# Optimization experiments

Measured on AMD Instinct MI355X. Metric: run time of the kernel, lower is better.

The kernel has to match this reference:

```python
import jax, jax.numpy as jnp
import numpy as np

D = 1024   # dim == seq_len L (forced by final proj on [L, L])
N = 16     # SSM state size
K = 3      # conv kernel size, padding=1 -> same length


def setup_inputs() -> dict:
    key = jax.random.key(0)
    ks = jax.random.split(key, 8)
    s = lambda k, shape, sc: (jax.random.normal(k, shape, jnp.float32) * sc)
    return {
        "x": s(ks[0], (2, D, D), 1.0),
        "W_proj": s(ks[1], (D, D), D ** -0.5),
        "b_proj": jnp.zeros((D,), jnp.float32),
        "conv_w": s(ks[2], (D, D, K), (D * K) ** -0.5),  # [out_ch, in_ch, K]
        "conv_b": jnp.zeros((D,), jnp.float32),
        "A_log": jnp.log(jnp.tile(jnp.arange(1, N + 1, dtype=jnp.float32)[None, :], (D, 1))),  # [D, N]
        "W_delta": s(ks[3], (D, D), D ** -0.5),
        "W_B": s(ks[4], (D, N), D ** -0.5),
        "W_C": s(ks[5], (D, N), D ** -0.5),
    }


def _ssm(x, A_log, W_delta, W_B, W_C):
    # Mamba S6 diagonal selective scan. x: [L, D]
    delta = jax.nn.softplus(x @ W_delta)            # [L, D]
    B = x @ W_B                                      # [L, N]
    C = x @ W_C                                      # [L, N]
    A = -jnp.exp(A_log)                              # [D, N]
    Abar = jnp.exp(delta[:, :, None] * A[None])      # [L, D, N]
    Bx = (delta * x)[:, :, None] * B[:, None, :]     # [L, D, N]

    def combine(e1, e2):
        a1, b1 = e1
        a2, b2 = e2
        return a1 * a2, a2 * b1 + b2

    _, h = jax.lax.associative_scan(combine, (Abar, Bx), axis=0)  # h: [L, D, N]
    return jnp.einsum('ldn,ln->ld', h, C)            # [L, D]


def reference(x, W_proj, b_proj, conv_w, conv_b, A_log, W_delta, W_B, W_C):
    p = x @ W_proj.T + b_proj                        # shared proj; [2, L, D]
    xm, xg = p[0], p[1]                              # mirrors `x, x_ = self.proj(x)` unpacking batch==2
    xg = jax.nn.silu(xg)                             # [L, D]
    # Conv1d treats xm as (channels=L, length=D), padding=1 -> same length
    xc = jax.lax.conv_general_dilated(
        xm[None], conv_w, window_strides=(1,), padding=[(1, 1)],
        dimension_numbers=('NCW', 'OIW', 'NCW'))[0] + conv_b[:, None]  # [L, D]
    xc = jax.nn.silu(xc)
    y = _ssm(xc, A_log, W_delta, W_B, W_C)           # [L, D]
    y = y @ xg.T                                     # [L, L]  (x @ x_.transpose(-1,-2))
    return y @ W_proj.T + b_proj                     # final shared proj; [L, L]
```

## Files before the change

### kernel.cpp

```cpp
#include <hip/hip_runtime.h>
#include <math.h>


#define LL 1024
#define DD 1024
#define NS 16
#define CCH 16
#define CLEN 64

typedef short     bf16x8_t __attribute__((ext_vector_type(8)));
typedef float     f32x4_t  __attribute__((ext_vector_type(4)));
typedef unsigned short u16x4_t __attribute__((ext_vector_type(4)));
typedef unsigned short u16x8_t __attribute__((ext_vector_type(8)));

__device__ __forceinline__ float silu_f(float x) { return x / (1.f + expf(-x)); }
__device__ __forceinline__ float softplus_f(float x) {
  return fmaxf(x, 0.f) + log1pf(expf(-fabsf(x)));
}
__device__ __forceinline__ unsigned short f2bf(float f) {
  unsigned int u = __float_as_uint(f);
  u += 0x7fffu + ((u >> 16) & 1u);
  return (unsigned short)(u >> 16);
}

template<int N> __device__ __forceinline__ void s_wait_vmcnt() {
  asm volatile("s_waitcnt vmcnt(%0)" :: "n"(N) : "memory");
}
__device__ __forceinline__ void raw_barrier() {
  asm volatile("s_barrier" ::: "memory");
}

__global__ __launch_bounds__(256) void castk(const float* __restrict__ in,
                                             unsigned short* __restrict__ out, int n) {
  int i = (blockIdx.x * 256 + threadIdx.x) * 4;
  if (i >= n) return;
  float4 v = *(const float4*)(in + i);
  u16x4_t o; o[0] = f2bf(v.x); o[1] = f2bf(v.y); o[2] = f2bf(v.z); o[3] = f2bf(v.w);
  *(u16x4_t*)(out + i) = o;
}

__global__ __launch_bounds__(256) void tcastk(const float* __restrict__ W,
                                              unsigned short* __restrict__ out) {
  __shared__ float T[64][65];
  const int t = threadIdx.x;
  const int r = t >> 2, cq = (t & 3) << 4;
  const int d0 = blockIdx.x * 64, k0 = blockIdx.y * 64;
  #pragma unroll
  for (int c = 0; c < 16; c += 4) {
    float4 v = *(const float4*)&W[(size_t)(k0 + r) * DD + d0 + cq + c];
    T[r][cq + c + 0] = v.x; T[r][cq + c + 1] = v.y;
    T[r][cq + c + 2] = v.z; T[r][cq + c + 3] = v.w;
  }
  __syncthreads();
  u16x8_t o0, o1;
  #pragma unroll
  for (int j = 0; j < 8; ++j) o0[j] = f2bf(T[cq + j][r]);
  #pragma unroll
  for (int j = 0; j < 8; ++j) o1[j] = f2bf(T[cq + 8 + j][r]);
  *(u16x8_t*)&out[(size_t)(d0 + r) * DD + k0 + cq] = o0;
  *(u16x8_t*)&out[(size_t)(d0 + r) * DD + k0 + cq + 8] = o1;
}

__global__ __launch_bounds__(256) void bct_cast(const float* __restrict__ WB,
                                                const float* __restrict__ WC,
                                                unsigned short* __restrict__ wcomb) {
  const int b = blockIdx.x;
  const int k = threadIdx.x * 4;
  u16x4_t o;
  if (b < 32) {
    const float* W = (b < 16) ? WB : WC;
    const int n = b & 15;
    #pragma unroll
    for (int j = 0; j < 4; ++j) o[j] = f2bf(W[(size_t)(k + j) * NS + n]);
  } else {
    o[0] = o[1] = o[2] = o[3] = 0;
  }
  *(u16x4_t*)&wcomb[(size_t)(1024 + b) * DD + k] = o;
}

__global__ __launch_bounds__(256) void transpose_f32(const float* __restrict__ in,
                                                     float* __restrict__ out) {
  __shared__ float T[64][65];
  const int t = threadIdx.x;
  const int r = t >> 4;
  const int cq = (t & 15) << 2;
  const int r0 = blockIdx.y * 64, c0 = blockIdx.x * 64;
  #pragma unroll
  for (int rr = 0; rr < 64; rr += 16) {
    float4 v = *(const float4*)&in[(size_t)(r0 + r + rr) * DD + c0 + cq];
    T[r + rr][cq + 0] = v.x; T[r + rr][cq + 1] = v.y;
    T[r + rr][cq + 2] = v.z; T[r + rr][cq + 3] = v.w;
  }
  __syncthreads();
  #pragma unroll
  for (int rr = 0; rr < 64; rr += 16) {
    float4 o;
    o.x = T[cq + 0][r + rr]; o.y = T[cq + 1][r + rr];
    o.z = T[cq + 2][r + rr]; o.w = T[cq + 3][r + rr];
    *(float4*)&out[(size_t)(c0 + r + rr) * LL + r0 + cq] = o;
  }
}

__global__ __launch_bounds__(256) void build_xsht(const unsigned short* __restrict__ xm,
                                                  unsigned short* __restrict__ out) {
  __shared__ unsigned short Xs[64][66];
  const int t = threadIdx.x;
  const int w0 = blockIdx.x * 64, i0 = blockIdx.y * 64;
  {
    const int r = t >> 2, cq = (t & 3) << 4;
    #pragma unroll
    for (int c = 0; c < 16; c += 4) {
      u16x4_t v = *(const u16x4_t*)&xm[(size_t)(i0 + r) * DD + w0 + cq + c];
      Xs[r][1 + cq + c + 0] = v[0]; Xs[r][1 + cq + c + 1] = v[1];
      Xs[r][1 + cq + c + 2] = v[2]; Xs[r][1 + cq + c + 3] = v[3];
    }
  }
  if (t < 64)                 Xs[t][0]       = (w0 > 0)        ? xm[(size_t)(i0 + t) * DD + w0 - 1]  : (unsigned short)0;
  else if (t < 128) { int r = t - 64; Xs[r][65] = (w0 + 64 < DD) ? xm[(size_t)(i0 + r) * DD + w0 + 64] : (unsigned short)0; }
  __syncthreads();
  const int wr = t >> 2, q = t & 3;
  unsigned short vals[48];
  #pragma unroll
  for (int ii = 0; ii < 16; ++ii)
    #pragma unroll
    for (int k = 0; k < 3; ++k)
      vals[ii * 3 + k] = Xs[q * 16 + ii][wr + k];
  #pragma unroll
  for (int s = 0; s < 6; ++s) {
    u16x8_t o;
    #pragma unroll
    for (int j = 0; j < 8; ++j) o[j] = vals[s * 8 + j];
    *(u16x8_t*)&out[(size_t)(w0 + wr) * 3072 + (size_t)i0 * 3 + q * 48 + s * 8] = o;
  }
}

template<int TM, int NC, int ACT, bool BROW, bool O32, bool O16>
__global__ __launch_bounds__(256) void gemm_bf16(
    const unsigned short* __restrict__ A, const unsigned short* __restrict__ B,
    const float* __restrict__ bias, float* __restrict__ C32,
    unsigned short* __restrict__ C16, int M, int N, int K)
{
  constexpr int MI   = TM / 32;
  constexpr int NI   = NC / 32;
  constexpr int ROWS = TM + NC;
  constexpr int GI   = ROWS * 8 / 256;
  __shared__ unsigned short s[3][ROWS * 64];
  const int tid  = threadIdx.x;
  const int lane = tid & 63;
  const int wv   = tid >> 6;
  const int wm   = wv >> 1, wn = wv & 1;
  const int m0 = blockIdx.y * TM, n0 = blockIdx.x * NC;
  const int wbase = tid & 192;

  f32x4_t acc[MI][NI];
  #pragma unroll
  for (int i = 0; i < MI; ++i)
    #pragma unroll
    for (int j = 0; j < NI; ++j)
      acc[i][j] = (f32x4_t)(0.f);

  auto stage = [&](int buf, int k0) {
    #pragma unroll
    for (int it = 0; it < GI; ++it) {
      const int c   = (it << 8) + tid;
      const int r   = c >> 3;
      const int kcg = (c & 7) ^ (r & 7);
      const unsigned short* src = (r < TM)
          ? (A + (size_t)(m0 + r) * K + k0 + kcg * 8)
          : (B + (size_t)(n0 + r - TM) * K + k0 + kcg * 8);
      __builtin_amdgcn_global_load_lds(
          (const __attribute__((address_space(1))) void*)src,
          (__attribute__((address_space(3))) void*)(&s[buf][0] + (size_t)((it << 8) + wbase) * 8),
          16, 0, 0);
    }
  };

  const int NT = K >> 6;
  stage(0, 0);
  stage(1, 64);
  s_wait_vmcnt<GI>();
  raw_barrier();

  for (int t = 0; t < NT; ++t) {
    if (t + 2 < NT) stage((t + 2) % 3, (t + 2) << 6);

    const unsigned short* sb = &s[t % 3][0];
    const int rl = lane & 15, kq = lane >> 4;
    bf16x8_t af[MI][2], bfr[NI][2];
    #pragma unroll
    for (int mi = 0; mi < MI; ++mi) {
      const int row = wm * (TM / 2) + mi * 16 + rl;
      #pragma unroll
      for (int ks = 0; ks < 2; ++ks) {
        const int ch = row * 8 + ((ks * 4 + kq) ^ (row & 7));
        af[mi][ks] = *(const bf16x8_t*)(sb + (size_t)ch * 8);
      }
    }
    #pragma unroll
    for (int ni = 0; ni < NI; ++ni) {
      const int row = TM + wn * (NC / 2) + ni * 16 + rl;
      #pragma unroll
      for (int ks = 0; ks < 2; ++ks) {
        const int ch = row * 8 + ((ks * 4 + kq) ^ (row & 7));
        bfr[ni][ks] = *(const bf16x8_t*)(sb + (size_t)ch * 8);
      }
    }
    #pragma unroll
    for (int mi = 0; mi < MI; ++mi)
      #pragma unroll
      for (int ni = 0; ni < NI; ++ni)
        #pragma unroll
        for (int ks = 0; ks < 2; ++ks)
          acc[mi][ni] = __builtin_amdgcn_mfma_f32_16x16x32_bf16(
              af[mi][ks], bfr[ni][ks], acc[mi][ni], 0, 0, 0);

    if (t + 1 < NT) {
      if (t + 2 < NT) s_wait_vmcnt<GI>();
      else            s_wait_vmcnt<0>();
      raw_barrier();
    }
  }

  const int rl = lane & 15, rg = lane >> 4;
  #pragma unroll
  for (int mi = 0; mi < MI; ++mi) {
    #pragma unroll
    for (int ni = 0; ni < NI; ++ni) {
      const int col = n0 + wn * (NC / 2) + ni * 16 + rl;
      #pragma unroll
      for (int j = 0; j < 4; ++j) {
        const int row = m0 + wm * (TM / 2) + mi * 16 + rg * 4 + j;
        float v = acc[mi][ni][j];
        if (bias) v += BROW ? bias[row] : bias[col];
        if (ACT == 1) v = silu_f(v);
        else if (ACT == 2) v = softplus_f(v);
        else if (ACT == 3) { if (row >= 1024) v = silu_f(v); }
        else if (ACT == 4) { if (row < 1024)  v = softplus_f(v); }
        if (O32) C32[(size_t)row * N + col] = v;
        if (O16) C16[(size_t)row * N + col] = f2bf(v);
      }
    }
  }
}

__global__ __launch_bounds__(256) void scan_p1(
    const float* __restrict__ deltaT, const float* __restrict__ xcT,
    const float* __restrict__ BT, const float* __restrict__ A_log,
    float* __restrict__ P, float* __restrict__ H)
{
  const int tid = threadIdx.x;
  const int n = tid & 15, dl = tid >> 4;
  const int d = blockIdx.y * 16 + dl;
  const int c = blockIdx.x;
  const int l0 = c * CLEN;
  const float Av = -expf(A_log[d * NS + n]);
  float h = 0.f, p = 1.f;
  for (int j = 0; j < CLEN; j += 4) {
    const float4 dv = *(const float4*)&deltaT[(size_t)d * LL + l0 + j];
    const float4 xv = *(const float4*)&xcT[(size_t)d * LL + l0 + j];
    const float4 bv = *(const float4*)&BT[(size_t)n * LL + l0 + j];
    const float dvu[4] = {dv.x, dv.y, dv.z, dv.w};
    const float xvu[4] = {xv.x, xv.y, xv.z, xv.w};
    const float bvu[4] = {bv.x, bv.y, bv.z, bv.w};
    #pragma unroll
    for (int u = 0; u < 4; ++u) {
      const float ab = expf(dvu[u] * Av);
      h = fmaf(ab, h, dvu[u] * xvu[u] * bvu[u]);
      p *= ab;
    }
  }
  const int idx = d * NS + n;
  P[(size_t)c * (DD * NS) + idx] = p;
  H[(size_t)c * (DD * NS) + idx] = h;
}

__global__ __launch_bounds__(256) void scan_p2(const float* __restrict__ P,
                                               const float* __restrict__ H,
                                               float* __restrict__ Hin) {
  const int idx = blockIdx.x * 256 + threadIdx.x;
  float hin = 0.f;
  Hin[idx] = 0.f;
  #pragma unroll
  for (int c = 1; c < CCH; ++c) {
    hin = fmaf(P[(size_t)(c - 1) * (DD * NS) + idx], hin,
               H[(size_t)(c - 1) * (DD * NS) + idx]);
    Hin[(size_t)c * (DD * NS) + idx] = hin;
  }
}

__global__ __launch_bounds__(256) void scan_p3(
    const float* __restrict__ deltaT, const float* __restrict__ xcT,
    const float* __restrict__ BT, const float* __restrict__ CT,
    const float* __restrict__ Hin, const float* __restrict__ A_log,
    unsigned short* __restrict__ y16)
{
  const int tid = threadIdx.x;
  const int n = tid & 15, dl = tid >> 4;
  const int d = blockIdx.y * 16 + dl;
  const int c = blockIdx.x;
  const int l0 = c * CLEN;
  const float Av = -expf(A_log[d * NS + n]);
  float h = Hin[(size_t)c * (DD * NS) + d * NS + n];
  for (int j = 0; j < CLEN; j += 4) {
    const float4 dv = *(const float4*)&deltaT[(size_t)d * LL + l0 + j];
    const float4 xv = *(const float4*)&xcT[(size_t)d * LL + l0 + j];
    const float4 bv = *(const float4*)&BT[(size_t)n * LL + l0 + j];
    const float4 cv = *(const float4*)&CT[(size_t)n * LL + l0 + j];
    const float dvu[4] = {dv.x, dv.y, dv.z, dv.w};
    const float xvu[4] = {xv.x, xv.y, xv.z, xv.w};
    const float bvu[4] = {bv.x, bv.y, bv.z, bv.w};
    const float cvu[4] = {cv.x, cv.y, cv.z, cv.w};
    #pragma unroll
    for (int u = 0; u < 4; ++u) {
      const int l = l0 + j + u;
      const float ab = expf(dvu[u] * Av);
      h = fmaf(ab, h, dvu[u] * xvu[u] * bvu[u]);
      float contrib = h * cvu[u];
      contrib += __shfl_xor(contrib, 1);
      contrib += __shfl_xor(contrib, 2);
      contrib += __shfl_xor(contrib, 4);
      contrib += __shfl_xor(contrib, 8);
      if (n == 0) y16[(size_t)l * DD + d] = f2bf(contrib);
    }
  }
}

extern "C" void kernel_launch(void* const* d_in, const int* in_sizes, int n_in,
                              void* d_out, int out_size, void* d_ws, size_t ws_size,
                              hipStream_t stream) {
  const float* x       = (const float*)d_in[0];
  const float* W_proj  = (const float*)d_in[1];
  const float* b_proj  = (const float*)d_in[2];
  const float* conv_w  = (const float*)d_in[3];
  const float* conv_b  = (const float*)d_in[4];
  const float* A_log   = (const float*)d_in[5];
  const float* W_delta = (const float*)d_in[6];
  const float* W_B     = (const float*)d_in[7];
  const float* W_C     = (const float*)d_in[8];
  float* out = (float*)d_out;

  char* w = (char*)d_ws;
  const size_t MB = 1024 * 1024;
  unsigned short* x16     = (unsigned short*)(w + 0);
  unsigned short* wp16    = (unsigned short*)(w + 4 * MB);
  unsigned short* cw16    = (unsigned short*)(w + 6 * MB);
  unsigned short* wcomb16 = (unsigned short*)(w + 12 * MB);
  unsigned short* pbuf    = (unsigned short*)(w + 15 * MB);
  unsigned short* xm16    = pbuf;
  unsigned short* xg16    = pbuf + 1024 * 1024;
  unsigned short* xsht    = (unsigned short*)(w + 19 * MB);
  unsigned short* xc16    = (unsigned short*)(w + 25 * MB);
  float*          xc32    = (float*)(w + 27 * MB);
  float*          xcT32   = (float*)(w + 31 * MB);
  float*          dcomb32 = (float*)(w + 35 * MB);
  float*          deltaT32= dcomb32;
  float*          BT32    = dcomb32 + (size_t)1024 * 1024;
  float*          CT32    = dcomb32 + (size_t)1040 * 1024;
  unsigned short* y16     = (unsigned short*)(w + 40 * MB);
  float*          Pc      = (float*)(w + 42 * MB);
  float*          Hc      = (float*)(w + 43 * MB);
  float*          HinC    = (float*)(w + 44 * MB);
  unsigned short* out116  = (unsigned short*)(w + 45 * MB);
  (void)ws_size;

  const dim3 blk(256);

  castk<<<dim3(2048), blk, 0, stream>>>(x, x16, 2 * 1024 * 1024);
  castk<<<dim3(1024), blk, 0, stream>>>(W_proj, wp16, 1024 * 1024);
  castk<<<dim3(3072), blk, 0, stream>>>(conv_w, cw16, 3 * 1024 * 1024);
  tcastk<<<dim3(16, 16), blk, 0, stream>>>(W_delta, wcomb16);
  bct_cast<<<dim3(64), blk, 0, stream>>>(W_B, W_C, wcomb16);

  gemm_bf16<64, 64, 3, false, false, true><<<dim3(16, 32), blk, 0, stream>>>(
      x16, wp16, b_proj, nullptr, pbuf, 2048, 1024, 1024);
  build_xsht<<<dim3(16, 16), blk, 0, stream>>>(xm16, xsht);
  gemm_bf16<64, 64, 1, true, true, true><<<dim3(16, 16), blk, 0, stream>>>(
      cw16, xsht, conv_b, xc32, xc16, 1024, 1024, 3072);
  gemm_bf16<64, 64, 4, false, true, false><<<dim3(16, 17), blk, 0, stream>>>(
      wcomb16, xc16, nullptr, dcomb32, nullptr, 1088, 1024, 1024);
  transpose_f32<<<dim3(16, 16), blk, 0, stream>>>(xc32, xcT32);
  scan_p1<<<dim3(CCH, DD / 16), blk, 0, stream>>>(deltaT32, xcT32, BT32, A_log, Pc, Hc);
  scan_p2<<<dim3(64), blk, 0, stream>>>(Pc, Hc, HinC);
  scan_p3<<<dim3(CCH, DD / 16), blk, 0, stream>>>(deltaT32, xcT32, BT32, CT32, HinC, A_log, y16);
  gemm_bf16<64, 64, 0, false, false, true><<<dim3(16, 16), blk, 0, stream>>>(
      y16, xg16, nullptr, nullptr, out116, 1024, 1024, 1024);
  gemm_bf16<64, 64, 0, false, true, false><<<dim3(16, 16), blk, 0, stream>>>(
      out116, wp16, b_proj, out, nullptr, 1024, 1024, 1024);
}
```

Measured before the change: 204.6 us.

## Replace 64x64 GEMMs with 128x128 split-K GEMMs plus fused reduction epilogues

```diff
diff --git a/kernel.cpp b/kernel.cpp
--- a/kernel.cpp
+++ b/kernel.cpp
@@ -78,29 +78,6 @@
   *(u16x4_t*)&wcomb[(size_t)(1024 + b) * DD + k] = o;
 }
 
-__global__ __launch_bounds__(256) void transpose_f32(const float* __restrict__ in,
-                                                     float* __restrict__ out) {
-  __shared__ float T[64][65];
-  const int t = threadIdx.x;
-  const int r = t >> 4;
-  const int cq = (t & 15) << 2;
-  const int r0 = blockIdx.y * 64, c0 = blockIdx.x * 64;
-  #pragma unroll
-  for (int rr = 0; rr < 64; rr += 16) {
-    float4 v = *(const float4*)&in[(size_t)(r0 + r + rr) * DD + c0 + cq];
-    T[r + rr][cq + 0] = v.x; T[r + rr][cq + 1] = v.y;
-    T[r + rr][cq + 2] = v.z; T[r + rr][cq + 3] = v.w;
-  }
-  __syncthreads();
-  #pragma unroll
-  for (int rr = 0; rr < 64; rr += 16) {
-    float4 o;
-    o.x = T[cq + 0][r + rr]; o.y = T[cq + 1][r + rr];
-    o.z = T[cq + 2][r + rr]; o.w = T[cq + 3][r + rr];
-    *(float4*)&out[(size_t)(c0 + r + rr) * LL + r0 + cq] = o;
-  }
-}
-
 __global__ __launch_bounds__(256) void build_xsht(const unsigned short* __restrict__ xm,
                                                   unsigned short* __restrict__ out) {
   __shared__ unsigned short Xs[64][66];
@@ -134,40 +111,36 @@
   }
 }
 
-template<int TM, int NC, int ACT, bool BROW, bool O32, bool O16>
-__global__ __launch_bounds__(256) void gemm_bf16(
+__global__ __launch_bounds__(256) void gemm_sk(
     const unsigned short* __restrict__ A, const unsigned short* __restrict__ B,
-    const float* __restrict__ bias, float* __restrict__ C32,
-    unsigned short* __restrict__ C16, int M, int N, int K)
+    float* __restrict__ part, size_t sliceStride, int N, int K, int Ksl)
 {
-  constexpr int MI   = TM / 32;
-  constexpr int NI   = NC / 32;
-  constexpr int ROWS = TM + NC;
-  constexpr int GI   = ROWS * 8 / 256;
-  __shared__ unsigned short s[3][ROWS * 64];
+  constexpr int GI = 4;
+  __shared__ unsigned short s[3][256 * 32];
   const int tid  = threadIdx.x;
   const int lane = tid & 63;
   const int wv   = tid >> 6;
   const int wm   = wv >> 1, wn = wv & 1;
-  const int m0 = blockIdx.y * TM, n0 = blockIdx.x * NC;
+  const int m0 = blockIdx.y * 128, n0 = blockIdx.x * 128;
   const int wbase = tid & 192;
-
-  f32x4_t acc[MI][NI];
-  #pragma unroll
-  for (int i = 0; i < MI; ++i)
-    #pragma unroll
-    for (int j = 0; j < NI; ++j)
+  const int koff = blockIdx.z * Ksl;
+
+  f32x4_t acc[4][4];
+  #pragma unroll
+  for (int i = 0; i < 4; ++i)
+    #pragma unroll
+    for (int j = 0; j < 4; ++j)
       acc[i][j] = (f32x4_t)(0.f);
 
-  auto stage = [&](int buf, int k0) {
+  auto stage = [&](int buf, int kbase) {
     #pragma unroll
     for (int it = 0; it < GI; ++it) {
       const int c   = (it << 8) + tid;
-      const int r   = c >> 3;
-      const int kcg = (c & 7) ^ (r & 7);
-      const unsigned short* src = (r < TM)
-          ? (A + (size_t)(m0 + r) * K + k0 + kcg * 8)
-          : (B + (size_t)(n0 + r - TM) * K + k0 + kcg * 8);
+      const int r   = c >> 2;
+      const int kcg = (c & 3) ^ ((r >> 1) & 3);
+      const unsigned short* src = (r < 128)
+          ? (A + (size_t)(m0 + r) * K + kbase + kcg * 8)
+          : (B + (size_t)(n0 + r - 128) * K + kbase + kcg * 8);
       __builtin_amdgcn_global_load_lds(
           (const __attribute__((address_space(1))) void*)src,
           (__attribute__((address_space(3))) void*)(&s[buf][0] + (size_t)((it << 8) + wbase) * 8),
@@ -175,44 +148,35 @@
     }
   };
 
-  const int NT = K >> 6;
-  stage(0, 0);
-  stage(1, 64);
+  const int NT = Ksl >> 5;
+  stage(0, koff);
+  stage(1, koff + 32);
   s_wait_vmcnt<GI>();
   raw_barrier();
 
   for (int t = 0; t < NT; ++t) {
-    if (t + 2 < NT) stage((t + 2) % 3, (t + 2) << 6);
+    if (t + 2 < NT) stage((t + 2) % 3, koff + (t + 2) * 32);
 
     const unsigned short* sb = &s[t % 3][0];
     const int rl = lane & 15, kq = lane >> 4;
-    bf16x8_t af[MI][2], bfr[NI][2];
-    #pragma unroll
-    for (int mi = 0; mi < MI; ++mi) {
-      const int row = wm * (TM / 2) + mi * 16 + rl;
+    bf16x8_t af[4], bfr[4];
+    #pragma unroll
+    for (int mi = 0; mi < 4; ++mi) {
+      const int row = wm * 64 + mi * 16 + rl;
+      const int ch  = row * 4 + (kq ^ ((row >> 1) & 3));
+      af[mi] = *(const bf16x8_t*)(sb + (size_t)ch * 8);
+    }
+    #pragma unroll
+    for (int ni = 0; ni < 4; ++ni) {
+      const int row = 128 + wn * 64 + ni * 16 + rl;
+      const int ch  = row * 4 + (kq ^ ((row >> 1) & 3));
+      bfr[ni] = *(const bf16x8_t*)(sb + (size_t)ch * 8);
+    }
+    #pragma unroll
+    for (int mi = 0; mi < 4; ++mi)
       #pragma unroll
-      for (int ks = 0; ks < 2; ++ks) {
-        const int ch = row * 8 + ((ks * 4 + kq) ^ (row & 7));
-        af[mi][ks] = *(const bf16x8_t*)(sb + (size_t)ch * 8);
-      }
-    }
-    #pragma unroll
-    for (int ni = 0; ni < NI; ++ni) {
-      const int row = TM + wn * (NC / 2) + ni * 16 + rl;
-      #pragma unroll
-      for (int ks = 0; ks < 2; ++ks) {
-        const int ch = row * 8 + ((ks * 4 + kq) ^ (row & 7));
-        bfr[ni][ks] = *(const bf16x8_t*)(sb + (size_t)ch * 8);
-      }
-    }
-    #pragma unroll
-    for (int mi = 0; mi < MI; ++mi)
-      #pragma unroll
-      for (int ni = 0; ni < NI; ++ni)
-        #pragma unroll
-        for (int ks = 0; ks < 2; ++ks)
-          acc[mi][ni] = __builtin_amdgcn_mfma_f32_16x16x32_bf16(
-              af[mi][ks], bfr[ni][ks], acc[mi][ni], 0, 0, 0);
+      for (int ni = 0; ni < 4; ++ni)
+        acc[mi][ni] = __builtin_amdgcn_mfma_f32_16x16x32_bf16(af[mi], bfr[ni], acc[mi][ni], 0, 0, 0);
 
     if (t + 1 < NT) {
       if (t + 2 < NT) s_wait_vmcnt<GI>();
@@ -221,25 +185,88 @@
     }
   }
 
+  float* pz = part + (size_t)blockIdx.z * sliceStride;
   const int rl = lane & 15, rg = lane >> 4;
   #pragma unroll
-  for (int mi = 0; mi < MI; ++mi) {
-    #pragma unroll
-    for (int ni = 0; ni < NI; ++ni) {
-      const int col = n0 + wn * (NC / 2) + ni * 16 + rl;
+  for (int mi = 0; mi < 4; ++mi) {
+    #pragma unroll
+    for (int ni = 0; ni < 4; ++ni) {
+      const int col = n0 + wn * 64 + ni * 16 + rl;
       #pragma unroll
       for (int j = 0; j < 4; ++j) {
-        const int row = m0 + wm * (TM / 2) + mi * 16 + rg * 4 + j;
-        float v = acc[mi][ni][j];
-        if (bias) v += BROW ? bias[row] : bias[col];
-        if (ACT == 1) v = silu_f(v);
-        else if (ACT == 2) v = softplus_f(v);
-        else if (ACT == 3) { if (row >= 1024) v = silu_f(v); }
-        else if (ACT == 4) { if (row < 1024)  v = softplus_f(v); }
-        if (O32) C32[(size_t)row * N + col] = v;
-        if (O16) C16[(size_t)row * N + col] = f2bf(v);
+        const int row = m0 + wm * 64 + mi * 16 + rg * 4 + j;
+        pz[(size_t)row * N + col] = acc[mi][ni][j];
       }
     }
+  }
+}
+
+template<int SK, int ACT, bool O32, bool O16>
+__global__ __launch_bounds__(256) void reduce_k(
+    const float* __restrict__ part, size_t sliceStride,
+    const float* __restrict__ bias,
+    float* __restrict__ C32, unsigned short* __restrict__ C16)
+{
+  const size_t idx = ((size_t)blockIdx.x * 256 + threadIdx.x) * 4;
+  const int row = (int)(idx >> 10), col = (int)(idx & 1023);
+  float4 s = *(const float4*)&part[idx];
+  #pragma unroll
+  for (int z = 1; z < SK; ++z) {
+    const float4 p = *(const float4*)&part[(size_t)z * sliceStride + idx];
+    s.x += p.x; s.y += p.y; s.z += p.z; s.w += p.w;
+  }
+  float v[4] = {s.x, s.y, s.z, s.w};
+  if (bias) {
+    const float4 bv = *(const float4*)&bias[col];
+    v[0] += bv.x; v[1] += bv.y; v[2] += bv.z; v[3] += bv.w;
+  }
+  #pragma unroll
+  for (int j = 0; j < 4; ++j) {
+    if (ACT == 2) v[j] = softplus_f(v[j]);
+    else if (ACT == 3) { if (row >= 1024) v[j] = silu_f(v[j]); }
+    else if (ACT == 4) { if (row < 1024)  v[j] = softplus_f(v[j]); }
+  }
+  if (O32) { float4 o; o.x = v[0]; o.y = v[1]; o.z = v[2]; o.w = v[3];
+             *(float4*)&C32[idx] = o; }
+  if (O16) { u16x4_t o; o[0] = f2bf(v[0]); o[1] = f2bf(v[1]);
+             o[2] = f2bf(v[2]); o[3] = f2bf(v[3]);
+             *(u16x4_t*)&C16[idx] = o; }
+}
+
+__global__ __launch_bounds__(256) void reduce_conv_t(
+    const float* __restrict__ part, const float* __restrict__ cb,
+    unsigned short* __restrict__ xc16, float* __restrict__ xcT)
+{
+  __shared__ float T[64][65];
+  const int t = threadIdx.x;
+  const int r = t >> 4;
+  const int cq = (t & 15) << 2;
+  const int r0 = blockIdx.y * 64, c0 = blockIdx.x * 64;
+  #pragma unroll
+  for (int rr = 0; rr < 64; rr += 16) {
+    const int row = r0 + r + rr;
+    const size_t base = (size_t)row * 1024 + c0 + cq;
+    float4 s = *(const float4*)&part[base];
+    #pragma unroll
+    for (int z = 1; z < 4; ++z) {
+      const float4 p = *(const float4*)&part[(size_t)z * (1024 * 1024) + base];
+      s.x += p.x; s.y += p.y; s.z += p.z; s.w += p.w;
+    }
+    const float b = cb[row];
+    float v[4] = {silu_f(s.x + b), silu_f(s.y + b), silu_f(s.z + b), silu_f(s.w + b)};
+    u16x4_t o16; o16[0] = f2bf(v[0]); o16[1] = f2bf(v[1]);
+    o16[2] = f2bf(v[2]); o16[3] = f2bf(v[3]);
+    *(u16x4_t*)&xc16[base] = o16;
+    T[r + rr][cq + 0] = v[0]; T[r + rr][cq + 1] = v[1];
+    T[r + rr][cq + 2] = v[2]; T[r + rr][cq + 3] = v[3];
+  }
+  __syncthreads();
+  #pragma unroll
+  for (int rr = 0; rr < 64; rr += 16) {
+    float4 o;
+    o.x = T[cq + 0][r + rr]; o.y = T[cq + 1][r + rr];
+    o.z = T[cq + 2][r + rr]; o.w = T[cq + 3][r + rr];
+    *(float4*)&xcT[(size_t)(c0 + r + rr) * LL + r0 + cq] = o;
   }
 }
 
@@ -340,27 +367,27 @@
   float* out = (float*)d_out;
 
   char* w = (char*)d_ws;
-  const size_t MB = 1024 * 1024;
-  unsigned short* x16     = (unsigned short*)(w + 0);
-  unsigned short* wp16    = (unsigned short*)(w + 4 * MB);
-  unsigned short* cw16    = (unsigned short*)(w + 6 * MB);
-  unsigned short* wcomb16 = (unsigned short*)(w + 12 * MB);
-  unsigned short* pbuf    = (unsigned short*)(w + 15 * MB);
+  const size_t QMB = 256 * 1024;
+  unsigned short* wp16    = (unsigned short*)(w);
+  unsigned short* pbuf    = (unsigned short*)(w + 8  * QMB);
   unsigned short* xm16    = pbuf;
   unsigned short* xg16    = pbuf + 1024 * 1024;
-  unsigned short* xsht    = (unsigned short*)(w + 19 * MB);
-  unsigned short* xc16    = (unsigned short*)(w + 25 * MB);
-  float*          xc32    = (float*)(w + 27 * MB);
-  float*          xcT32   = (float*)(w + 31 * MB);
-  float*          dcomb32 = (float*)(w + 35 * MB);
+  unsigned short* wcomb16 = (unsigned short*)(w + 24 * QMB);
+  unsigned short* xc16    = (unsigned short*)(w + 34 * QMB);
+  float*          xcT32   = (float*)(w + 42 * QMB);
+  unsigned short* x16     = (unsigned short*)(w + 58 * QMB);
+  float*          dcomb32 = (float*)(w + 58 * QMB);
   float*          deltaT32= dcomb32;
   float*          BT32    = dcomb32 + (size_t)1024 * 1024;
   float*          CT32    = dcomb32 + (size_t)1040 * 1024;
-  unsigned short* y16     = (unsigned short*)(w + 40 * MB);
-  float*          Pc      = (float*)(w + 42 * MB);
-  float*          Hc      = (float*)(w + 43 * MB);
-  float*          HinC    = (float*)(w + 44 * MB);
-  unsigned short* out116  = (unsigned short*)(w + 45 * MB);
+  unsigned short* cw16    = (unsigned short*)(w + 75 * QMB);
+  unsigned short* y16     = (unsigned short*)(w + 75 * QMB);
+  float*          Pc      = (float*)(w + 83 * QMB);
+  float*          Hc      = (float*)(w + 87 * QMB);
+  float*          HinC    = (float*)(w + 91 * QMB);
+  unsigned short* out116  = (unsigned short*)(w + 87 * QMB);
+  unsigned short* xsht    = (unsigned short*)(w + 99 * QMB);
+  float*          part    = (float*)(w + 123 * QMB);
   (void)ws_size;
 
   const dim3 blk(256);
@@ -369,21 +396,29 @@
   castk<<<dim3(1024), blk, 0, stream>>>(W_proj, wp16, 1024 * 1024);
   castk<<<dim3(3072), blk, 0, stream>>>(conv_w, cw16, 3 * 1024 * 1024);
   tcastk<<<dim3(16, 16), blk, 0, stream>>>(W_delta, wcomb16);
-  bct_cast<<<dim3(64), blk, 0, stream>>>(W_B, W_C, wcomb16);
-
-  gemm_bf16<64, 64, 3, false, false, true><<<dim3(16, 32), blk, 0, stream>>>(
-      x16, wp16, b_proj, nullptr, pbuf, 2048, 1024, 1024);
+  bct_cast<<<dim3(128), blk, 0, stream>>>(W_B, W_C, wcomb16);
+
+  gemm_sk<<<dim3(8, 16, 2), blk, 0, stream>>>(x16, wp16, part,
+      (size_t)2048 * 1024, 1024, 1024, 512);
+  reduce_k<2, 3, false, true><<<dim3(2048), blk, 0, stream>>>(
+      part, (size_t)2048 * 1024, b_proj, nullptr, pbuf);
   build_xsht<<<dim3(16, 16), blk, 0, stream>>>(xm16, xsht);
-  gemm_bf16<64, 64, 1, true, true, true><<<dim3(16, 16), blk, 0, stream>>>(
-      cw16, xsht, conv_b, xc32, xc16, 1024, 1024, 3072);
-  gemm_bf16<64, 64, 4, false, true, false><<<dim3(16, 17), blk, 0, stream>>>(
-      wcomb16, xc16, nullptr, dcomb32, nullptr, 1088, 1024, 1024);
-  transpose_f32<<<dim3(16, 16), blk, 0, stream>>>(xc32, xcT32);
+  gemm_sk<<<dim3(8, 8, 4), blk, 0, stream>>>(cw16, xsht, part,
+      (size_t)1024 * 1024, 1024, 3072, 768);
+  reduce_conv_t<<<dim3(16, 16), blk, 0, stream>>>(part, conv_b, xc16, xcT32);
+  gemm_sk<<<dim3(8, 9, 2), blk, 0, stream>>>(wcomb16, xc16, part,
+      (size_t)1152 * 1024, 1024, 1024, 512);
+  reduce_k<2, 4, true, false><<<dim3(1056), blk, 0, stream>>>(
+      part, (size_t)1152 * 1024, nullptr, dcomb32, nullptr);
   scan_p1<<<dim3(CCH, DD / 16), blk, 0, stream>>>(deltaT32, xcT32, BT32, A_log, Pc, Hc);
   scan_p2<<<dim3(64), blk, 0, stream>>>(Pc, Hc, HinC);
   scan_p3<<<dim3(CCH, DD / 16), blk, 0, stream>>>(deltaT32, xcT32, BT32, CT32, HinC, A_log, y16);
-  gemm_bf16<64, 64, 0, false, false, true><<<dim3(16, 16), blk, 0, stream>>>(
-      y16, xg16, nullptr, nullptr, out116, 1024, 1024, 1024);
-  gemm_bf16<64, 64, 0, false, true, false><<<dim3(16, 16), blk, 0, stream>>>(
-      out116, wp16, b_proj, out, nullptr, 1024, 1024, 1024);
-}
+  gemm_sk<<<dim3(8, 8, 4), blk, 0, stream>>>(y16, xg16, part,
+      (size_t)1024 * 1024, 1024, 1024, 256);
+  reduce_k<4, 0, false, true><<<dim3(1024), blk, 0, stream>>>(
+      part, (size_t)1024 * 1024, nullptr, nullptr, out116);
+  gemm_sk<<<dim3(8, 8, 4), blk, 0, stream>>>(out116, wp16, part,
+      (size_t)1024 * 1024, 1024, 1024, 256);
+  reduce_k<4, 0, true, false><<<dim3(1024), blk, 0, stream>>>(
+      part, (size_t)1024 * 1024, b_proj, out, nullptr);
+}
```

Result: slower. 225.2 us (+10.1%).
